# Kernel optimization log

Measured on AMD Instinct MI355X. Metric: run time of the kernel, lower is better.

Reference implementation:

```python
import jax, jax.numpy as jnp
import numpy as np

L, B, T, C = 4, 4, 2048, 1024
FFN = 4 * C
STD = 0.02
EPS = 1e-5
NEG_INF = -1e38


def setup_inputs() -> dict:
    key = jax.random.key(0)
    ks = jax.random.split(key, 18)
    n = lambda k, shape, s=STD: jax.random.normal(k, shape, jnp.float32) * s
    u = lambda k, shape: jax.random.uniform(k, shape, jnp.float32)
    return {
        "x": jax.random.normal(ks[0], (B, T, C), jnp.float32),
        "ln1_w": jnp.ones((L, C), jnp.float32),
        "tm_mix_k": u(ks[1], (L, 1, 1, C)),
        "tm_mix_v": u(ks[2], (L, 1, 1, C)),
        "tm_mix_r": u(ks[3], (L, 1, 1, C)),
        "tm_k_w": n(ks[4], (L, C, C)),
        "tm_v_w": n(ks[5], (L, C, C)),
        "tm_r_w": n(ks[6], (L, C, C)),
        "tm_o_w": n(ks[7], (L, C, C)),
        # time_decay in [-5, 1] like RWKV decay_speed init; w = -exp(time_decay)
        "time_decay": u(ks[8], (L, C)) * 6.0 - 5.0,
        "time_first": jnp.log(0.3).astype(jnp.float32) + 0.5 * jax.random.normal(ks[9], (L, C), jnp.float32),
        "ln2_w": jnp.ones((L, C), jnp.float32),
        "cm_mix_k": u(ks[10], (L, 1, 1, C)),
        "cm_mix_r": u(ks[11], (L, 1, 1, C)),
        "cm_k_w": n(ks[12], (L, FFN, C)),
        "cm_v_w": n(ks[13], (L, C, FFN)),
        "cm_r_w": n(ks[14], (L, C, C)),
        "lnf_w": jnp.ones((C,), jnp.float32),
    }


def layer_norm(x, w):
    mu = jnp.mean(x, axis=-1, keepdims=True)
    var = jnp.mean(jnp.square(x - mu), axis=-1, keepdims=True)
    return (x - mu) * jax.lax.rsqrt(var + EPS) * w


def time_shift(x):
    # ZeroPad2d((0,0,1,-1)): shift sequence right by one, zero at t=0
    return jnp.pad(x, ((0, 0), (1, 0), (0, 0)))[:, :-1]


def wkv_scan(k, v, time_decay, time_first):
    # k, v: [B, T, C]; numerically-stabilized linear WKV recurrence over T
    w = -jnp.exp(time_decay)  # [C]
    u = time_first            # [C]
    zeros = jnp.zeros(k.shape[::2], k.dtype)  # [B, C]

    def step(carry, kv):
        num, den, mx = carry
        kt, vt = kv
        max_out = jnp.maximum(mx, kt + u)
        e1 = jnp.exp(mx - max_out)
        e2 = jnp.exp(kt + u - max_out)
        out = (e1 * num + e2 * vt) / (e1 * den + e2)
        max_st = jnp.maximum(mx + w, kt)
        e1 = jnp.exp(mx + w - max_st)
        e2 = jnp.exp(kt - max_st)
        return (e1 * num + e2 * vt, e1 * den + e2, max_st), out

    init = (zeros, zeros, jnp.full_like(zeros, NEG_INF))
    _, out = jax.lax.scan(step, init, (k.swapaxes(0, 1), v.swapaxes(0, 1)))
    return out.swapaxes(0, 1)  # [B, T, C]


def reference(x, ln1_w, tm_mix_k, tm_mix_v, tm_mix_r, tm_k_w, tm_v_w, tm_r_w, tm_o_w,
              time_decay, time_first, ln2_w, cm_mix_k, cm_mix_r, cm_k_w, cm_v_w, cm_r_w, lnf_w):
    n_layer = ln1_w.shape[0]
    for l in range(n_layer):
        # --- TimeMixing ---
        h = layer_norm(x, ln1_w[l])
        prev = time_shift(h)
        k = jnp.einsum('btc,oc->bto', h * tm_mix_k[l] + prev * (1 - tm_mix_k[l]), tm_k_w[l])
        v = jnp.einsum('btc,oc->bto', h * tm_mix_v[l] + prev * (1 - tm_mix_v[l]), tm_v_w[l])
        r = jax.nn.sigmoid(jnp.einsum('btc,oc->bto', h * tm_mix_r[l] + prev * (1 - tm_mix_r[l]), tm_r_w[l]))
        wkv = wkv_scan(k, v, time_decay[l], time_first[l])
        x = x + jnp.einsum('btc,oc->bto', r * wkv, tm_o_w[l])
        # --- ChannelMixing ---
        h = layer_norm(x, ln2_w[l])
        prev = time_shift(h)
        kk = jnp.einsum('btc,fc->btf', h * cm_mix_k[l] + prev * (1 - cm_mix_k[l]), cm_k_w[l])  # [B,T,4C]
        vv = jnp.einsum('btf,of->bto', jnp.square(jax.nn.relu(kk)), cm_v_w[l])
        rr = jax.nn.sigmoid(jnp.einsum('btc,oc->bto', h * cm_mix_r[l] + prev * (1 - cm_mix_r[l]), cm_r_w[l]))
        x = x + rr * vv
    return layer_norm(x, lnf_w)
```

## Files before the change

kernel.cpp:

```cpp
#include <hip/hip_runtime.h>
#include <hip/hip_bf16.h>


#define LNUM 4
#define BSZ  4
#define TSZ  2048
#define CSZ  1024
#define FFND 4096
#define MROWS (BSZ*TSZ)
#define EPSF 1e-5f

typedef __hip_bfloat16 bf16;
typedef __bf16 bf16x8 __attribute__((ext_vector_type(8)));
typedef float f32x4 __attribute__((ext_vector_type(4)));

#define BM 128
#define BN 128
#define BK 64

#define SCK  64
#define SLEN (TSZ/SCK)

__device__ __forceinline__ void async_copy16(const void* g, void* l) {
    __builtin_amdgcn_global_load_lds((const __attribute__((address_space(1))) void*)g,
                                     (__attribute__((address_space(3))) void*)l, 16, 0, 0);
}

template<int MODE>
__launch_bounds__(256)
__global__ void gemm_bt(const bf16* __restrict__ A, const bf16* __restrict__ Bw,
                        void* __restrict__ outp, const float* __restrict__ aux,
                        int K, int N)
{
    __shared__ __align__(16) __bf16 sA[BM*BK];
    __shared__ __align__(16) __bf16 sB[BN*BK];
    const int tid  = threadIdx.x;
    const int lane = tid & 63;
    const int wid  = tid >> 6;
    const int wm   = wid >> 1;
    const int wn   = wid & 1;
    const size_t bm0 = (size_t)blockIdx.x * BM;
    const size_t bn0 = (size_t)blockIdx.y * BN;

    const int lrow8 = lane >> 3;
    const int cbl   = lane & 7;
    const int cbg   = cbl ^ lrow8;

    const bf16* pA[4]; const bf16* pB[4];
#pragma unroll
    for (int i = 0; i < 4; ++i) {
        const int rg = (i*4 + wid) * 8;
        pA[i] = A  + (bm0 + rg + lrow8) * (size_t)K + cbg*8;
        pB[i] = Bw + (bn0 + rg + lrow8) * (size_t)K + cbg*8;
    }

    f32x4 acc[4][4];
#pragma unroll
    for (int a = 0; a < 4; ++a)
#pragma unroll
        for (int b = 0; b < 4; ++b) acc[a][b] = (f32x4){0.f,0.f,0.f,0.f};

    const int q   = lane >> 4;
    const int rlo = lane & 15;

    const int ktiles = K / BK;
    for (int kt = 0; kt < ktiles; ++kt) {
#pragma unroll
        for (int i = 0; i < 4; ++i) {
            const int rg = (i*4 + wid) * 8;
            async_copy16(pA[i], &sA[rg*BK]);
            async_copy16(pB[i], &sB[rg*BK]);
            pA[i] += BK; pB[i] += BK;
        }
        __syncthreads();
#pragma unroll
        for (int ks = 0; ks < 2; ++ks) {
            bf16x8 aF[4], bF[4];
#pragma unroll
            for (int mt = 0; mt < 4; ++mt) {
                const int r  = wm*64 + mt*16 + rlo;
                const int cb = (ks*4 + q) ^ (r & 7);
                aF[mt] = *(const bf16x8*)&sA[r*BK + cb*8];
            }
#pragma unroll
            for (int nt = 0; nt < 4; ++nt) {
                const int r  = wn*64 + nt*16 + rlo;
                const int cb = (ks*4 + q) ^ (r & 7);
                bF[nt] = *(const bf16x8*)&sB[r*BK + cb*8];
            }
#pragma unroll
            for (int mt = 0; mt < 4; ++mt)
#pragma unroll
                for (int nt = 0; nt < 4; ++nt)
                    acc[mt][nt] = __builtin_amdgcn_mfma_f32_16x16x32_bf16(
                        aF[mt], bF[nt], acc[mt][nt], 0, 0, 0);
        }
        __syncthreads();
    }

#pragma unroll
    for (int mt = 0; mt < 4; ++mt) {
#pragma unroll
        for (int nt = 0; nt < 4; ++nt) {
            const size_t col = bn0 + wn*64 + nt*16 + rlo;
#pragma unroll
            for (int i = 0; i < 4; ++i) {
                const size_t row = bm0 + wm*64 + mt*16 + q*4 + i;
                const size_t idx = row * (size_t)N + col;
                const float v = acc[mt][nt][i];
                if (MODE == 0) {
                    ((bf16*)outp)[idx] = __float2bfloat16(v);
                } else if (MODE == 1) {
                    ((bf16*)outp)[idx] = __float2bfloat16(1.f/(1.f+__expf(-v)));
                } else if (MODE == 2) {
                    ((float*)outp)[idx] += v;
                } else if (MODE == 3) {
                    const float t = fmaxf(v, 0.f);
                    ((bf16*)outp)[idx] = __float2bfloat16(t*t);
                } else if (MODE == 4) {
                    ((float*)outp)[idx] = 1.f/(1.f+__expf(-v));
                } else {
                    ((float*)outp)[idx] += aux[idx] * v;
                }
            }
        }
    }
}

template<int NOUT>
__launch_bounds__(256)
__global__ void ln_mix_kernel(const float* __restrict__ x, const float* __restrict__ lnw,
                              const float* __restrict__ mka, const float* __restrict__ mva,
                              const float* __restrict__ mra,
                              bf16* __restrict__ ok, bf16* __restrict__ ov, bf16* __restrict__ orr)
{
    const int bt  = blockIdx.x;
    const int t   = bt % TSZ;
    const int tid = threadIdx.x;
    const float4 xc = ((const float4*)(x + (size_t)bt*CSZ))[tid];
    float4 xp = {0.f,0.f,0.f,0.f};
    const bool hasp = (t != 0);
    if (hasp) xp = ((const float4*)(x + (size_t)(bt-1)*CSZ))[tid];

    float s0 = xc.x+xc.y+xc.z+xc.w;
    float s1 = xc.x*xc.x+xc.y*xc.y+xc.z*xc.z+xc.w*xc.w;
    float s2 = xp.x+xp.y+xp.z+xp.w;
    float s3 = xp.x*xp.x+xp.y*xp.y+xp.z*xp.z+xp.w*xp.w;
#pragma unroll
    for (int off = 32; off > 0; off >>= 1) {
        s0 += __shfl_down(s0, off); s1 += __shfl_down(s1, off);
        s2 += __shfl_down(s2, off); s3 += __shfl_down(s3, off);
    }
    __shared__ float red[4][4];
    if ((tid & 63) == 0) { const int wq = tid >> 6;
        red[wq][0]=s0; red[wq][1]=s1; red[wq][2]=s2; red[wq][3]=s3; }
    __syncthreads();
    s0 = red[0][0]+red[1][0]+red[2][0]+red[3][0];
    s1 = red[0][1]+red[1][1]+red[2][1]+red[3][1];
    s2 = red[0][2]+red[1][2]+red[2][2]+red[3][2];
    s3 = red[0][3]+red[1][3]+red[2][3]+red[3][3];

    const float inv = 1.f/CSZ;
    const float muC = s0*inv;
    const float rsC = rsqrtf(s1*inv - muC*muC + EPSF);
    const float muP = s2*inv;
    const float rsP = rsqrtf(s3*inv - muP*muP + EPSF);

    const int c4 = tid*4;
    const float4 lw = ((const float4*)lnw)[tid];
    const float4 mk = ((const float4*)mka)[tid];
    const float4 mv = (NOUT >= 2) ? ((const float4*)mva)[tid] : lw;
    const float4 mr = (NOUT >= 3) ? ((const float4*)mra)[tid] : lw;

    float hcv[4] = {(xc.x-muC)*rsC*lw.x, (xc.y-muC)*rsC*lw.y,
                    (xc.z-muC)*rsC*lw.z, (xc.w-muC)*rsC*lw.w};
    float hpv[4];
    if (hasp) {
        hpv[0]=(xp.x-muP)*rsP*lw.x; hpv[1]=(xp.y-muP)*rsP*lw.y;
        hpv[2]=(xp.z-muP)*rsP*lw.z; hpv[3]=(xp.w-muP)*rsP*lw.w;
    } else { hpv[0]=hpv[1]=hpv[2]=hpv[3]=0.f; }
    const float mkv[4]={mk.x,mk.y,mk.z,mk.w};
    const float mvv[4]={mv.x,mv.y,mv.z,mv.w};
    const float mrv[4]={mr.x,mr.y,mr.z,mr.w};

    __align__(8) bf16 o0[4], o1[4], o2[4];
#pragma unroll
    for (int j = 0; j < 4; ++j) {
        o0[j] = __float2bfloat16(hcv[j]*mkv[j] + hpv[j]*(1.f-mkv[j]));
        if (NOUT >= 2) o1[j] = __float2bfloat16(hcv[j]*mvv[j] + hpv[j]*(1.f-mvv[j]));
        if (NOUT >= 3) o2[j] = __float2bfloat16(hcv[j]*mrv[j] + hpv[j]*(1.f-mrv[j]));
    }
    *(uint2*)(ok + (size_t)bt*CSZ + c4) = *(const uint2*)o0;
    if (NOUT >= 2) *(uint2*)(ov  + (size_t)bt*CSZ + c4) = *(const uint2*)o1;
    if (NOUT >= 3) *(uint2*)(orr + (size_t)bt*CSZ + c4) = *(const uint2*)o2;
}


__launch_bounds__(256)
__global__ void wkv_sum_kernel(const bf16* __restrict__ kb, const bf16* __restrict__ vb,
                               const float* __restrict__ td,
                               float* __restrict__ sN, float* __restrict__ sD,
                               float* __restrict__ sM)
{
    const int j  = blockIdx.x;
    const int b  = blockIdx.y >> 2;
    const int cg = blockIdx.y & 3;
    const int c  = cg*256 + threadIdx.x;
    const float w = -__expf(td[c]);

    size_t idx = ((size_t)b*TSZ + j*SLEN)*CSZ + c;
    float num = 0.f, den = 0.f, mx = -1e38f;
    float kt = (float)kb[idx], vt = (float)vb[idx];
    for (int t = 0; t < SLEN; ++t) {
        float kn = 0.f, vn = 0.f;
        if (t + 1 < SLEN) {
            kn = (float)kb[idx + CSZ]; vn = (float)vb[idx + CSZ];
        }
        const float ms = fmaxf(mx + w, kt);
        const float p1 = __expf(mx + w - ms);
        const float p2 = __expf(kt - ms);
        num = p1*num + p2*vt; den = p1*den + p2; mx = ms;
        idx += CSZ; kt = kn; vt = vn;
    }
    const size_t sidx = ((size_t)b*SCK + j)*CSZ + c;
    sN[sidx] = num; sD[sidx] = den; sM[sidx] = mx;
}

__launch_bounds__(256)
__global__ void wkv_comb_kernel(const float* __restrict__ td,
                                float* __restrict__ sN, float* __restrict__ sD,
                                float* __restrict__ sM)
{
    const int id = blockIdx.x*256 + threadIdx.x;
    const int b  = id >> 10;
    const int c  = id & (CSZ-1);
    const float wL = -__expf(td[c]) * (float)SLEN;
    float n = 0.f, d = 0.f, m = -1e38f;
    size_t idx = (size_t)b*SCK*CSZ + c;
    float nl = sN[idx], dl = sD[idx], ml = sM[idx];
    for (int j = 0; j < SCK; ++j) {
        float nn = 0.f, dn = 0.f, mn = 0.f;
        if (j + 1 < SCK) {
            nn = sN[idx + CSZ]; dn = sD[idx + CSZ]; mn = sM[idx + CSZ];
        }
        sN[idx] = n; sD[idx] = d; sM[idx] = m;
        const float mi = m + wL;
        const float mo = fmaxf(mi, ml);
        const float e1 = __expf(mi - mo);
        const float e2 = __expf(ml - mo);
        n = e1*n + e2*nl; d = e1*d + e2*dl; m = mo;
        idx += CSZ; nl = nn; dl = dn; ml = mn;
    }
}

__launch_bounds__(256)
__global__ void wkv_out_kernel(const bf16* __restrict__ kb, const bf16* __restrict__ vb,
                               const bf16* __restrict__ rb,
                               const float* __restrict__ td, const float* __restrict__ tf,
                               const float* __restrict__ sN, const float* __restrict__ sD,
                               const float* __restrict__ sM,
                               bf16* __restrict__ outb)
{
    const int j  = blockIdx.x;
    const int b  = blockIdx.y >> 2;
    const int cg = blockIdx.y & 3;
    const int c  = cg*256 + threadIdx.x;
    const float w = -__expf(td[c]);
    const float u = tf[c];

    const size_t sidx = ((size_t)b*SCK + j)*CSZ + c;
    float num = sN[sidx], den = sD[sidx], mx = sM[sidx];

    size_t idx = ((size_t)b*TSZ + j*SLEN)*CSZ + c;
    float kt = (float)kb[idx], vt = (float)vb[idx], rt = (float)rb[idx];
    for (int t = 0; t < SLEN; ++t) {
        float kn = 0.f, vn = 0.f, rn = 0.f;
        if (t + 1 < SLEN) {
            kn = (float)kb[idx + CSZ]; vn = (float)vb[idx + CSZ]; rn = (float)rb[idx + CSZ];
        }
        const float ku = kt + u;
        const float mo = fmaxf(mx, ku);
        const float e1 = __expf(mx - mo);
        const float e2 = __expf(ku - mo);
        const float outv = (e1*num + e2*vt) / (e1*den + e2);
        const float ms = fmaxf(mx + w, kt);
        const float p1 = __expf(mx + w - ms);
        const float p2 = __expf(kt - ms);
        num = p1*num + p2*vt; den = p1*den + p2; mx = ms;
        outb[idx] = __float2bfloat16(rt * outv);
        idx += CSZ; kt = kn; vt = vn; rt = rn;
    }
}

__launch_bounds__(256)
__global__ void final_ln_kernel(const float* __restrict__ x, const float* __restrict__ lnw,
                                float* __restrict__ out)
{
    const int bt  = blockIdx.x;
    const int tid = threadIdx.x;
    const float4 xc = ((const float4*)(x + (size_t)bt*CSZ))[tid];
    float s0 = xc.x+xc.y+xc.z+xc.w;
    float s1 = xc.x*xc.x+xc.y*xc.y+xc.z*xc.z+xc.w*xc.w;
#pragma unroll
    for (int off = 32; off > 0; off >>= 1) {
        s0 += __shfl_down(s0, off); s1 += __shfl_down(s1, off);
    }
    __shared__ float red[4][2];
    if ((tid & 63) == 0) { red[tid>>6][0] = s0; red[tid>>6][1] = s1; }
    __syncthreads();
    s0 = red[0][0]+red[1][0]+red[2][0]+red[3][0];
    s1 = red[0][1]+red[1][1]+red[2][1]+red[3][1];
    const float inv = 1.f/CSZ;
    const float mu = s0*inv;
    const float rs = rsqrtf(s1*inv - mu*mu + EPSF);
    const float4 lw = ((const float4*)lnw)[tid];
    float4 o;
    o.x = (xc.x-mu)*rs*lw.x; o.y = (xc.y-mu)*rs*lw.y;
    o.z = (xc.z-mu)*rs*lw.z; o.w = (xc.w-mu)*rs*lw.w;
    ((float4*)(out + (size_t)bt*CSZ))[tid] = o;
}

#define N4_CC (CSZ*CSZ/4)
#define N4_FC (FFND*CSZ/4)
__global__ void cvt_weights_kernel(const float* __restrict__ tk, const float* __restrict__ tv,
                                   const float* __restrict__ tr, const float* __restrict__ to,
                                   const float* __restrict__ ck, const float* __restrict__ cv,
                                   const float* __restrict__ cr,
                                   bf16* __restrict__ wk, bf16* __restrict__ wv,
                                   bf16* __restrict__ wr, bf16* __restrict__ wo,
                                   bf16* __restrict__ wck, bf16* __restrict__ wcv,
                                   bf16* __restrict__ wcr)
{
    int i = blockIdx.x * 256 + threadIdx.x;
    const float* s; bf16* d;
    if      (i < 1*N4_CC)          { s = tk; d = wk;  }
    else if (i < 2*N4_CC)          { s = tv; d = wv;  i -= 1*N4_CC; }
    else if (i < 3*N4_CC)          { s = tr; d = wr;  i -= 2*N4_CC; }
    else if (i < 4*N4_CC)          { s = to; d = wo;  i -= 3*N4_CC; }
    else if (i < 4*N4_CC+N4_FC)    { s = ck; d = wck; i -= 4*N4_CC; }
    else if (i < 4*N4_CC+2*N4_FC)  { s = cv; d = wcv; i -= 4*N4_CC+N4_FC; }
    else                           { s = cr; d = wcr; i -= 4*N4_CC+2*N4_FC; }
    const float4 f = ((const float4*)s)[i];
    __align__(8) bf16 o[4] = {__float2bfloat16(f.x), __float2bfloat16(f.y),
                              __float2bfloat16(f.z), __float2bfloat16(f.w)};
    ((uint2*)d)[i] = *(const uint2*)o;
}
#define CVT_TOTAL4 (4*N4_CC + 2*N4_FC + N4_CC)

static constexpr size_t SZ_XF32 = (size_t)MROWS*CSZ*4;
static constexpr size_t SZ_ABF  = (size_t)MROWS*CSZ*2;
static constexpr size_t OFF_X   = 0;
static constexpr size_t OFF_XK  = OFF_X  + SZ_XF32;
static constexpr size_t OFF_XV  = OFF_XK + SZ_ABF;
static constexpr size_t OFF_XR  = OFF_XV + SZ_ABF;
static constexpr size_t OFF_K   = OFF_XR + SZ_ABF;
static constexpr size_t OFF_V   = OFF_K  + SZ_ABF;
static constexpr size_t OFF_R   = OFF_V  + SZ_ABF;
static constexpr size_t OFF_KK  = OFF_R  + SZ_ABF;
static constexpr size_t OFF_W   = OFF_KK + (size_t)MROWS*FFND*2;
static constexpr size_t OFF_WK  = OFF_W;
static constexpr size_t OFF_WV  = OFF_WK + (size_t)CSZ*CSZ*2;
static constexpr size_t OFF_WR  = OFF_WV + (size_t)CSZ*CSZ*2;
static constexpr size_t OFF_WO  = OFF_WR + (size_t)CSZ*CSZ*2;
static constexpr size_t OFF_WCK = OFF_WO + (size_t)CSZ*CSZ*2;
static constexpr size_t OFF_WCV = OFF_WCK + (size_t)FFND*CSZ*2;
static constexpr size_t OFF_WCR = OFF_WCV + (size_t)CSZ*FFND*2;

static constexpr size_t SZ_SUM  = (size_t)BSZ*SCK*CSZ*4;

extern "C" void kernel_launch(void* const* d_in, const int* in_sizes, int n_in,
                              void* d_out, int out_size, void* d_ws, size_t ws_size,
                              hipStream_t stream)
{
    const float* xin   = (const float*)d_in[0];
    const float* ln1w  = (const float*)d_in[1];
    const float* tmixk = (const float*)d_in[2];
    const float* tmixv = (const float*)d_in[3];
    const float* tmixr = (const float*)d_in[4];
    const float* tkw   = (const float*)d_in[5];
    const float* tvw   = (const float*)d_in[6];
    const float* trw   = (const float*)d_in[7];
    const float* tow   = (const float*)d_in[8];
    const float* tdec  = (const float*)d_in[9];
    const float* tfst  = (const float*)d_in[10];
    const float* ln2w  = (const float*)d_in[11];
    const float* cmixk = (const float*)d_in[12];
    const float* cmixr = (const float*)d_in[13];
    const float* ckw   = (const float*)d_in[14];
    const float* cvw   = (const float*)d_in[15];
    const float* crw   = (const float*)d_in[16];
    const float* lnfw  = (const float*)d_in[17];

    char* ws = (char*)d_ws;
    float* xres = (float*)(ws + OFF_X);
    bf16* xk  = (bf16*)(ws + OFF_XK);
    bf16* xv  = (bf16*)(ws + OFF_XV);
    bf16* xr  = (bf16*)(ws + OFF_XR);
    bf16* kb  = (bf16*)(ws + OFF_K);
    bf16* vb  = (bf16*)(ws + OFF_V);
    bf16* rb  = (bf16*)(ws + OFF_R);
    bf16* kkb = (bf16*)(ws + OFF_KK);
    bf16* rwkv = xk;
    float* rr  = (float*)(ws + OFF_K);
    float* sN  = (float*)(ws + OFF_KK);
    float* sD  = (float*)(ws + OFF_KK + SZ_SUM);
    float* sM  = (float*)(ws + OFF_KK + 2*SZ_SUM);
    bf16* wk  = (bf16*)(ws + OFF_WK);
    bf16* wv  = (bf16*)(ws + OFF_WV);
    bf16* wr  = (bf16*)(ws + OFF_WR);
    bf16* wo  = (bf16*)(ws + OFF_WO);
    bf16* wck = (bf16*)(ws + OFF_WCK);
    bf16* wcv = (bf16*)(ws + OFF_WCV);
    bf16* wcr = (bf16*)(ws + OFF_WCR);

    hipMemcpyAsync(xres, xin, SZ_XF32, hipMemcpyDeviceToDevice, stream);

    const dim3 blk(256);
    const dim3 gC(MROWS/BM, CSZ/BN);
    const dim3 gF(MROWS/BM, FFND/BN);
    const dim3 gScan(SCK, BSZ*4);

    for (int l = 0; l < LNUM; ++l) {
        const size_t oC  = (size_t)l*CSZ;
        const size_t oCC = (size_t)l*CSZ*CSZ;
        const size_t oFC = (size_t)l*FFND*CSZ;
        cvt_weights_kernel<<<CVT_TOTAL4/256, blk, 0, stream>>>(
            tkw + oCC, tvw + oCC, trw + oCC, tow + oCC,
            ckw + oFC, cvw + oFC, crw + oCC,
            wk, wv, wr, wo, wck, wcv, wcr);

        ln_mix_kernel<3><<<MROWS, blk, 0, stream>>>(xres, ln1w + oC,
            tmixk + oC, tmixv + oC, tmixr + oC, xk, xv, xr);
        gemm_bt<0><<<gC, blk, 0, stream>>>(xk, wk, kb, nullptr, CSZ, CSZ);
        gemm_bt<0><<<gC, blk, 0, stream>>>(xv, wv, vb, nullptr, CSZ, CSZ);
        gemm_bt<1><<<gC, blk, 0, stream>>>(xr, wr, rb, nullptr, CSZ, CSZ);
        wkv_sum_kernel<<<gScan, blk, 0, stream>>>(kb, vb, tdec + oC, sN, sD, sM);
        wkv_comb_kernel<<<(BSZ*CSZ)/256, blk, 0, stream>>>(tdec + oC, sN, sD, sM);
        wkv_out_kernel<<<gScan, blk, 0, stream>>>(kb, vb, rb, tdec + oC, tfst + oC,
            sN, sD, sM, rwkv);
        gemm_bt<2><<<gC, blk, 0, stream>>>(rwkv, wo, xres, nullptr, CSZ, CSZ);

        ln_mix_kernel<2><<<MROWS, blk, 0, stream>>>(xres, ln2w + oC,
            cmixk + oC, cmixr + oC, nullptr, xk, xv, nullptr);
        gemm_bt<3><<<gF, blk, 0, stream>>>(xk, wck, kkb, nullptr, CSZ, FFND);
        gemm_bt<4><<<gC, blk, 0, stream>>>(xv, wcr, rr, nullptr, CSZ, CSZ);
        gemm_bt<5><<<gC, blk, 0, stream>>>(kkb, wcv, xres, rr, FFND, CSZ);
    }
    final_ln_kernel<<<MROWS, blk, 0, stream>>>(xres, lnfw, (float*)d_out);
}
```

Measured before the change: 1.801 ms.

## Batch K/V/R projections into one launch and use narrower tiles for C-wide GEMMs

Merges the three time-mix projection GEMMs into a single kernel that picks its operands from the z grid dimension, and runs the C-output GEMMs with 128x64 tiles so each launch has twice as many blocks, giving more CUs work at M=8192, N=1024. The channel-mix receptance gate is now stored as bf16 instead of fp32, halving that buffer's traffic in the final fused GEMM at a small precision cost. Narrower tiles reduce reuse of the A tile and increase A-side load traffic.

New measurement: 1.668 ms. -7.4%, faster.

```diff
diff --git a/kernel.cpp b/kernel.cpp
--- a/kernel.cpp
+++ b/kernel.cpp
@@ -15,7 +15,6 @@
 typedef float f32x4 __attribute__((ext_vector_type(4)));
 
 #define BM 128
-#define BN 128
 #define BK 64
 
 #define SCK  64
@@ -26,37 +25,38 @@
                                      (__attribute__((address_space(3))) void*)l, 16, 0, 0);
 }
 
-template<int MODE>
+template<int MODE, int TBN>
 __launch_bounds__(256)
 __global__ void gemm_bt(const bf16* __restrict__ A, const bf16* __restrict__ Bw,
-                        void* __restrict__ outp, const float* __restrict__ aux,
+                        void* __restrict__ outp, const bf16* __restrict__ aux,
                         int K, int N)
 {
+    constexpr int MT  = (TBN == 128) ? 4 : 2;
+    constexpr int NBI = TBN / 32;
     __shared__ __align__(16) __bf16 sA[BM*BK];
-    __shared__ __align__(16) __bf16 sB[BN*BK];
+    __shared__ __align__(16) __bf16 sB[TBN*BK];
     const int tid  = threadIdx.x;
     const int lane = tid & 63;
     const int wid  = tid >> 6;
-    const int wm   = wid >> 1;
-    const int wn   = wid & 1;
+    const int wmB  = (TBN == 128) ? (wid >> 1) * 64 : wid * 32;
+    const int wnB  = (TBN == 128) ? (wid & 1) * 64 : 0;
     const size_t bm0 = (size_t)blockIdx.x * BM;
-    const size_t bn0 = (size_t)blockIdx.y * BN;
+    const size_t bn0 = (size_t)blockIdx.y * TBN;
 
     const int lrow8 = lane >> 3;
-    const int cbl   = lane & 7;
-    const int cbg   = cbl ^ lrow8;
-
-    const bf16* pA[4]; const bf16* pB[4];
-#pragma unroll
-    for (int i = 0; i < 4; ++i) {
-        const int rg = (i*4 + wid) * 8;
-        pA[i] = A  + (bm0 + rg + lrow8) * (size_t)K + cbg*8;
-        pB[i] = Bw + (bn0 + rg + lrow8) * (size_t)K + cbg*8;
-    }
-
-    f32x4 acc[4][4];
-#pragma unroll
-    for (int a = 0; a < 4; ++a)
+    const int cbg   = (lane & 7) ^ lrow8;
+
+    const bf16* pA[4]; const bf16* pB[NBI];
+#pragma unroll
+    for (int i = 0; i < 4; ++i)
+        pA[i] = A + (bm0 + (i*4 + wid)*8 + lrow8) * (size_t)K + cbg*8;
+#pragma unroll
+    for (int i = 0; i < NBI; ++i)
+        pB[i] = Bw + (bn0 + (i*4 + wid)*8 + lrow8) * (size_t)K + cbg*8;
+
+    f32x4 acc[MT][4];
+#pragma unroll
+    for (int a = 0; a < MT; ++a)
 #pragma unroll
         for (int b = 0; b < 4; ++b) acc[a][b] = (f32x4){0.f,0.f,0.f,0.f};
 
@@ -67,29 +67,32 @@
     for (int kt = 0; kt < ktiles; ++kt) {
 #pragma unroll
         for (int i = 0; i < 4; ++i) {
-            const int rg = (i*4 + wid) * 8;
-            async_copy16(pA[i], &sA[rg*BK]);
-            async_copy16(pB[i], &sB[rg*BK]);
-            pA[i] += BK; pB[i] += BK;
+            async_copy16(pA[i], &sA[(i*4 + wid)*8*BK]);
+            pA[i] += BK;
+        }
+#pragma unroll
+        for (int i = 0; i < NBI; ++i) {
+            async_copy16(pB[i], &sB[(i*4 + wid)*8*BK]);
+            pB[i] += BK;
         }
         __syncthreads();
 #pragma unroll
         for (int ks = 0; ks < 2; ++ks) {
-            bf16x8 aF[4], bF[4];
-#pragma unroll
-            for (int mt = 0; mt < 4; ++mt) {
-                const int r  = wm*64 + mt*16 + rlo;
+            bf16x8 aF[MT], bF[4];
+#pragma unroll
+            for (int mt = 0; mt < MT; ++mt) {
+                const int r  = wmB + mt*16 + rlo;
                 const int cb = (ks*4 + q) ^ (r & 7);
                 aF[mt] = *(const bf16x8*)&sA[r*BK + cb*8];
             }
 #pragma unroll
             for (int nt = 0; nt < 4; ++nt) {
-                const int r  = wn*64 + nt*16 + rlo;
+                const int r  = wnB + nt*16 + rlo;
                 const int cb = (ks*4 + q) ^ (r & 7);
                 bF[nt] = *(const bf16x8*)&sB[r*BK + cb*8];
             }
 #pragma unroll
-            for (int mt = 0; mt < 4; ++mt)
+            for (int mt = 0; mt < MT; ++mt)
 #pragma unroll
                 for (int nt = 0; nt < 4; ++nt)
                     acc[mt][nt] = __builtin_amdgcn_mfma_f32_16x16x32_bf16(
@@ -99,29 +102,121 @@
     }
 
 #pragma unroll
-    for (int mt = 0; mt < 4; ++mt) {
+    for (int mt = 0; mt < MT; ++mt) {
 #pragma unroll
         for (int nt = 0; nt < 4; ++nt) {
-            const size_t col = bn0 + wn*64 + nt*16 + rlo;
+            const size_t col = bn0 + wnB + nt*16 + rlo;
 #pragma unroll
             for (int i = 0; i < 4; ++i) {
-                const size_t row = bm0 + wm*64 + mt*16 + q*4 + i;
+                const size_t row = bm0 + wmB + mt*16 + q*4 + i;
                 const size_t idx = row * (size_t)N + col;
                 const float v = acc[mt][nt][i];
-                if (MODE == 0) {
-                    ((bf16*)outp)[idx] = __float2bfloat16(v);
-                } else if (MODE == 1) {
-                    ((bf16*)outp)[idx] = __float2bfloat16(1.f/(1.f+__expf(-v)));
-                } else if (MODE == 2) {
+                if (MODE == 2) {
                     ((float*)outp)[idx] += v;
                 } else if (MODE == 3) {
                     const float t = fmaxf(v, 0.f);
                     ((bf16*)outp)[idx] = __float2bfloat16(t*t);
                 } else if (MODE == 4) {
-                    ((float*)outp)[idx] = 1.f/(1.f+__expf(-v));
+                    ((bf16*)outp)[idx] = __float2bfloat16(1.f/(1.f+__expf(-v)));
                 } else {
-                    ((float*)outp)[idx] += aux[idx] * v;
+                    ((float*)outp)[idx] += (float)aux[idx] * v;
                 }
+            }
+        }
+    }
+}
+
+__launch_bounds__(256)
+__global__ void gemm_kvr(const bf16* __restrict__ A0, const bf16* __restrict__ A1,
+                         const bf16* __restrict__ A2,
+                         const bf16* __restrict__ W0, const bf16* __restrict__ W1,
+                         const bf16* __restrict__ W2,
+                         bf16* __restrict__ O0, bf16* __restrict__ O1,
+                         bf16* __restrict__ O2)
+{
+    constexpr int TBN = 64, MT = 2, NBI = 2, K = CSZ, N = CSZ;
+    const int z = blockIdx.z;
+    const bf16* A  = (z == 0) ? A0 : (z == 1) ? A1 : A2;
+    const bf16* Bw = (z == 0) ? W0 : (z == 1) ? W1 : W2;
+    bf16* outp     = (z == 0) ? O0 : (z == 1) ? O1 : O2;
+
+    __shared__ __align__(16) __bf16 sA[BM*BK];
+    __shared__ __align__(16) __bf16 sB[TBN*BK];
+    const int tid  = threadIdx.x;
+    const int lane = tid & 63;
+    const int wid  = tid >> 6;
+    const int wmB  = wid * 32;
+    const size_t bm0 = (size_t)blockIdx.x * BM;
+    const size_t bn0 = (size_t)blockIdx.y * TBN;
+
+    const int lrow8 = lane >> 3;
+    const int cbg   = (lane & 7) ^ lrow8;
+
+    const bf16* pA[4]; const bf16* pB[NBI];
+#pragma unroll
+    for (int i = 0; i < 4; ++i)
+        pA[i] = A + (bm0 + (i*4 + wid)*8 + lrow8) * (size_t)K + cbg*8;
+#pragma unroll
+    for (int i = 0; i < NBI; ++i)
+        pB[i] = Bw + (bn0 + (i*4 + wid)*8 + lrow8) * (size_t)K + cbg*8;
+
+    f32x4 acc[MT][4];
+#pragma unroll
+    for (int a = 0; a < MT; ++a)
+#pragma unroll
+        for (int b = 0; b < 4; ++b) acc[a][b] = (f32x4){0.f,0.f,0.f,0.f};
+
+    const int q   = lane >> 4;
+    const int rlo = lane & 15;
+
+    for (int kt = 0; kt < K/BK; ++kt) {
+#pragma unroll
+        for (int i = 0; i < 4; ++i) {
+            async_copy16(pA[i], &sA[(i*4 + wid)*8*BK]);
+            pA[i] += BK;
+        }
+#pragma unroll
+        for (int i = 0; i < NBI; ++i) {
+            async_copy16(pB[i], &sB[(i*4 + wid)*8*BK]);
+            pB[i] += BK;
+        }
+        __syncthreads();
+#pragma unroll
+        for (int ks = 0; ks < 2; ++ks) {
+            bf16x8 aF[MT], bF[4];
+#pragma unroll
+            for (int mt = 0; mt < MT; ++mt) {
+                const int r  = wmB + mt*16 + rlo;
+                const int cb = (ks*4 + q) ^ (r & 7);
+                aF[mt] = *(const bf16x8*)&sA[r*BK + cb*8];
+            }
+#pragma unroll
+            for (int nt = 0; nt < 4; ++nt) {
+                const int r  = nt*16 + rlo;
+                const int cb = (ks*4 + q) ^ (r & 7);
+                bF[nt] = *(const bf16x8*)&sB[r*BK + cb*8];
+            }
+#pragma unroll
+            for (int mt = 0; mt < MT; ++mt)
+#pragma unroll
+                for (int nt = 0; nt < 4; ++nt)
+                    acc[mt][nt] = __builtin_amdgcn_mfma_f32_16x16x32_bf16(
+                        aF[mt], bF[nt], acc[mt][nt], 0, 0, 0);
+        }
+        __syncthreads();
+    }
+
+#pragma unroll
+    for (int mt = 0; mt < MT; ++mt) {
+#pragma unroll
+        for (int nt = 0; nt < 4; ++nt) {
+            const size_t col = bn0 + nt*16 + rlo;
+#pragma unroll
+            for (int i = 0; i < 4; ++i) {
+                const size_t row = bm0 + wmB + mt*16 + q*4 + i;
+                float v = acc[mt][nt][i];
+                if (z == 2) v = 1.f/(1.f+__expf(-v));
+                ((bf16*)outp)[row * (size_t)N + col] = __float2bfloat16(v);
             }
         }
     }
@@ -194,7 +289,6 @@
     if (NOUT >= 2) *(uint2*)(ov  + (size_t)bt*CSZ + c4) = *(const uint2*)o1;
     if (NOUT >= 3) *(uint2*)(orr + (size_t)bt*CSZ + c4) = *(const uint2*)o2;
 }
-
 
 __launch_bounds__(256)
 __global__ void wkv_sum_kernel(const bf16* __restrict__ kb, const bf16* __restrict__ vb,
@@ -401,7 +495,7 @@
     bf16* rb  = (bf16*)(ws + OFF_R);
     bf16* kkb = (bf16*)(ws + OFF_KK);
     bf16* rwkv = xk;
-    float* rr  = (float*)(ws + OFF_K);
+    bf16* rr  = (bf16*)(ws + OFF_K);
     float* sN  = (float*)(ws + OFF_KK);
     float* sD  = (float*)(ws + OFF_KK + SZ_SUM);
     float* sM  = (float*)(ws + OFF_KK + 2*SZ_SUM);
@@ -416,8 +510,9 @@
     hipMemcpyAsync(xres, xin, SZ_XF32, hipMemcpyDeviceToDevice, stream);
 
     const dim3 blk(256);
-    const dim3 gC(MROWS/BM, CSZ/BN);
-    const dim3 gF(MROWS/BM, FFND/BN);
+    const dim3 gKVR(MROWS/BM, CSZ/64, 3);
+    const dim3 gC64(MROWS/BM, CSZ/64);
+    const dim3 gF(MROWS/BM, FFND/128);
     const dim3 gScan(SCK, BSZ*4);
 
     for (int l = 0; l < LNUM; ++l) {
@@ -431,20 +526,18 @@
 
         ln_mix_kernel<3><<<MROWS, blk, 0, stream>>>(xres, ln1w + oC,
             tmixk + oC, tmixv + oC, tmixr + oC, xk, xv, xr);
-        gemm_bt<0><<<gC, blk, 0, stream>>>(xk, wk, kb, nullptr, CSZ, CSZ);
-        gemm_bt<0><<<gC, blk, 0, stream>>>(xv, wv, vb, nullptr, CSZ, CSZ);
-        gemm_bt<1><<<gC, blk, 0, stream>>>(xr, wr, rb, nullptr, CSZ, CSZ);
+        gemm_kvr<<<gKVR, blk, 0, stream>>>(xk, xv, xr, wk, wv, wr, kb, vb, rb);
         wkv_sum_kernel<<<gScan, blk, 0, stream>>>(kb, vb, tdec + oC, sN, sD, sM);
         wkv_comb_kernel<<<(BSZ*CSZ)/256, blk, 0, stream>>>(tdec + oC, sN, sD, sM);
         wkv_out_kernel<<<gScan, blk, 0, stream>>>(kb, vb, rb, tdec + oC, tfst + oC,
             sN, sD, sM, rwkv);
-        gemm_bt<2><<<gC, blk, 0, stream>>>(rwkv, wo, xres, nullptr, CSZ, CSZ);
+        gemm_bt<2,64><<<gC64, blk, 0, stream>>>(rwkv, wo, xres, nullptr, CSZ, CSZ);
 
         ln_mix_kernel<2><<<MROWS, blk, 0, stream>>>(xres, ln2w + oC,
             cmixk + oC, cmixr + oC, nullptr, xk, xv, nullptr);
-        gemm_bt<3><<<gF, blk, 0, stream>>>(xk, wck, kkb, nullptr, CSZ, FFND);
-        gemm_bt<4><<<gC, blk, 0, stream>>>(xv, wcr, rr, nullptr, CSZ, CSZ);
-        gemm_bt<5><<<gC, blk, 0, stream>>>(kkb, wcv, xres, rr, FFND, CSZ);
+        gemm_bt<3,128><<<gF, blk, 0, stream>>>(xk, wck, kkb, nullptr, CSZ, FFND);
+        gemm_bt<4,64><<<gC64, blk, 0, stream>>>(xv, wcr, rr, nullptr, CSZ, CSZ);
+        gemm_bt<5,64><<<gC64, blk, 0, stream>>>(kkb, wcv, xres, rr, FFND, CSZ);
     }
     final_ln_kernel<<<MROWS, blk, 0, stream>>>(xres, lnfw, (float*)d_out);
 }
```
